# Kernel tuning notes

Measured on AMD Instinct MI355X. Metric: run time of the kernel, lower is better.

Reference implementation:

```python
import jax, jax.numpy as jnp
import numpy as np

EMBED_DIM = 128
NUM_SYMBOLS = 200000
B = 1024
K = 200
PROCESS_STEPS = 4


def setup_inputs() -> dict:
    key = jax.random.key(0)
    ks = jax.random.split(key, 10)
    D = EMBED_DIM
    emb = jax.random.normal(ks[0], (NUM_SYMBOLS + 1, D), jnp.float32) * 0.02
    emb = emb.at[NUM_SYMBOLS].set(0.0)  # padding_idx row
    return {
        "relations": jax.random.randint(ks[1], (B, K), 0, NUM_SYMBOLS),
        "entities": jax.random.randint(ks[2], (B, K), 0, NUM_SYMBOLS),
        "query": jax.random.randint(ks[3], (B,), 0, NUM_SYMBOLS),
        "symbol_emb": emb,
        "gcn_w_w": jax.random.normal(ks[4], (D, 2 * D), jnp.float32) / np.sqrt(2 * D).astype(np.float32),
        "gcn_w_b": jnp.zeros((D,), jnp.float32),
        "p1_w": jax.random.normal(ks[5], (2 * D, D), jnp.float32) / np.sqrt(D).astype(np.float32),
        "p1_b": jnp.zeros((2 * D,), jnp.float32),
        "p2_w": jax.random.normal(ks[6], (D, 2 * D), jnp.float32) / np.sqrt(2 * D).astype(np.float32),
        "p2_b": jnp.zeros((D,), jnp.float32),
        "ln_a": jnp.ones((D,), jnp.float32),
        "ln_b": jnp.zeros((D,), jnp.float32),
        "w_ih": jax.random.normal(ks[7], (8 * D, D), jnp.float32) * 0.05,
        "w_hh": jax.random.normal(ks[8], (8 * D, 2 * D), jnp.float32) * 0.05,
        "b_ih": jnp.zeros((8 * D,), jnp.float32),
        "b_hh": jnp.zeros((8 * D,), jnp.float32),
    }


def _layer_norm(z, a, b, eps=1e-3):
    # repo's LayerNormalization: (z - mu) / (std + eps) * a + b, unbiased std
    mu = jnp.mean(z, axis=-1, keepdims=True)
    sigma = jnp.std(z, axis=-1, ddof=1, keepdims=True)
    return (z - mu) / (sigma + eps) * a + b


def _forward(symbol_emb, gcn_w_w, gcn_w_b, p1_w, p1_b, p2_w, p2_b,
             ln_a, ln_b, w_ih, w_hh, b_ih, b_hh,
             relations, entities, query):
    D = symbol_emb.shape[1]
    # --- neighbor_encoder: gather -> concat -> linear -> neighbor sum -> tanh
    rel_e = symbol_emb[relations]                       # (B, K, D)
    ent_e = symbol_emb[entities]                        # (B, K, D)
    concat = jnp.concatenate([rel_e, ent_e], axis=-1)   # (B, K, 2D)
    out = jnp.einsum('bkf,df->bkd', concat, gcn_w_w) + gcn_w_b
    num_neighbors = jnp.asarray(relations.shape[0], out.dtype)  # code uses relations.size()[0]
    support = jnp.tanh(out.sum(axis=1) / num_neighbors)  # (B, D)
    # --- SupportEncoder: FFN with residual + layernorm (dropout off in eval)
    hidden = jax.nn.relu(support @ p1_w.T + p1_b)        # (B, 2D)
    support_g = _layer_norm(hidden @ p2_w.T + p2_b + support, ln_a, ln_b)
    # --- QueryEncoder: LSTMCell(D, 2D) process block with attention over support
    q = symbol_emb[query]                                # (B, D)
    bsz = q.shape[0]
    h_r = jnp.zeros((bsz, 2 * D), q.dtype)
    c = jnp.zeros((bsz, 2 * D), q.dtype)
    h_out = q
    for _ in range(PROCESS_STEPS):
        gates = q @ w_ih.T + b_ih + h_r @ w_hh.T + b_hh  # (B, 8D)
        i, f, g, o = jnp.split(gates, 4, axis=-1)
        c = jax.nn.sigmoid(f) * c + jax.nn.sigmoid(i) * jnp.tanh(g)
        h_ = jax.nn.sigmoid(o) * jnp.tanh(c)             # (B, 2D)
        h_out = q + h_[:, :D]                            # (B, D)
        attn = jax.nn.softmax(h_out @ support_g.T, axis=1)  # (B, B)
        r = attn @ support_g                             # (B, D)
        h_r = jnp.concatenate([h_out, r], axis=-1)       # (B, 2D)
    query_embeds = h_out
    # --- cosine similarity over dim=1
    cross = jnp.sum(query_embeds * support_g, axis=1)
    n1 = jnp.sum(query_embeds * query_embeds, axis=1)
    n2 = jnp.sum(support_g * support_g, axis=1)
    return cross / jnp.sqrt(n1 * n2)                     # (B,)


def reference(relations, entities, query, symbol_emb, gcn_w_w, gcn_w_b,
              p1_w, p1_b, p2_w, p2_b, ln_a, ln_b, w_ih, w_hh, b_ih, b_hh):
    return _forward(symbol_emb, gcn_w_w, gcn_w_b, p1_w, p1_b, p2_w, p2_b,
                    ln_a, ln_b, w_ih, w_hh, b_ih, b_hh,
                    relations, entities, query)
```

## Files before the change

### kernel.cpp

```cpp
#include <hip/hip_runtime.h>
#include <math.h>

#define D 128
#define B_SZ 1024
#define KNB 200
#define AW 392
#define SCW 1028
#define PW 1032

typedef _Float16 half8 __attribute__((ext_vector_type(8)));
typedef _Float16 half4 __attribute__((ext_vector_type(4)));
typedef float floatx4 __attribute__((ext_vector_type(4)));

__device__ __forceinline__ float sigmoid_f(float x) { return 1.f / (1.f + __expf(-x)); }
__device__ __forceinline__ float tanh_fast(float x) { return 1.f - 2.f / (__expf(2.f * x) + 1.f); }

__global__ __launch_bounds__(256) void k_prefetch(
    const float4* __restrict__ emb4, int n4, float* __restrict__ scratch)
{
    float s = 0.f;
    for (int i = blockIdx.x * 256 + threadIdx.x; i < n4; i += gridDim.x * 256) {
        float4 v = emb4[i];
        s += v.x + v.y + v.z + v.w;
    }
    for (int off = 32; off; off >>= 1) s += __shfl_down(s, off);
    if ((threadIdx.x & 63) == 0) scratch[blockIdx.x * 4 + (threadIdx.x >> 6)] = s;
}

__global__ __launch_bounds__(256) void k_cvtw(
    const float* __restrict__ w_ih, const float* __restrict__ w_hh,
    _Float16* __restrict__ w16)
{
    const int i8 = (blockIdx.x * 256 + threadIdx.x) * 8;
    const int row = i8 / 384, k = i8 % 384;
    const float* src = (k < 128) ? &w_ih[row * 128 + k] : &w_hh[row * 256 + (k - 128)];
    float4 v0 = *(const float4*)src;
    float4 v1 = *(const float4*)(src + 4);
    half8 h;
    h[0] = (_Float16)v0.x; h[1] = (_Float16)v0.y; h[2] = (_Float16)v0.z; h[3] = (_Float16)v0.w;
    h[4] = (_Float16)v1.x; h[5] = (_Float16)v1.y; h[6] = (_Float16)v1.z; h[7] = (_Float16)v1.w;
    *(half8*)&w16[i8] = h;
}

__global__ __launch_bounds__(512) void k_support(
    const int* __restrict__ relations, const int* __restrict__ entities,
    const int* __restrict__ query, const float* __restrict__ emb,
    const float* __restrict__ gcn_w, const float* __restrict__ gcn_b,
    const float* __restrict__ p1_w, const float* __restrict__ p1_b,
    const float* __restrict__ p2_w, const float* __restrict__ p2_b,
    const float* __restrict__ ln_a, const float* __restrict__ ln_b,
    float* __restrict__ sg, _Float16* __restrict__ sgH, _Float16* __restrict__ sgT,
    _Float16* __restrict__ qbH)
{
    __shared__ int idxs[2 * KNB];
    __shared__ __align__(16) float part[16][132];
    __shared__ __align__(16) float S[2 * D];
    __shared__ __align__(16) float sup[D];
    __shared__ __align__(16) float hid[2 * D];
    __shared__ __align__(16) float zv[D];
    __shared__ float red2[2];

    const int b = blockIdx.x;
    const int t = threadIdx.x;

    if (t < KNB) idxs[t] = relations[b * KNB + t];
    else if (t < 2 * KNB) idxs[t] = entities[b * KNB + (t - KNB)];
    __syncthreads();

    {
        const int g = t >> 5, c4 = (t & 31) * 4;
        const int* mi = &idxs[(g >> 3) * KNB];
        float4 a4 = make_float4(0.f, 0.f, 0.f, 0.f);
        #pragma unroll 5
        for (int k = (g & 7); k < KNB; k += 8) {
            float4 v = *(const float4*)&emb[(size_t)mi[k] * D + c4];
            a4.x += v.x; a4.y += v.y; a4.z += v.z; a4.w += v.w;
        }
        *(float4*)&part[g][c4] = a4;
    }
    __syncthreads();
    if (t < 2 * D) {
        const int half = t >> 7, c = t & 127;
        float s = 0.f;
        #pragma unroll
        for (int j = 0; j < 8; ++j) s += part[half * 8 + j][c];
        S[t] = s;
    }
    __syncthreads();

    if (t < D) {
        const float4* w4 = (const float4*)(gcn_w + t * 2 * D);
        float dot = 0.f;
        #pragma unroll 8
        for (int f = 0; f < 2 * D / 4; ++f) {
            float4 w = w4[f];
            float4 s = *(const float4*)&S[f * 4];
            dot += w.x * s.x + w.y * s.y + w.z * s.z + w.w * s.w;
        }
        float v = (dot + 200.f * gcn_b[t]) * (1.f / 1024.f);
        sup[t] = tanhf(v);
    }
    __syncthreads();

    if (t < 2 * D) {
        const float4* w4 = (const float4*)(p1_w + t * D);
        float dot = 0.f;
        #pragma unroll 8
        for (int f = 0; f < D / 4; ++f) {
            float4 w = w4[f];
            float4 s = *(const float4*)&sup[f * 4];
            dot += w.x * s.x + w.y * s.y + w.z * s.z + w.w * s.w;
        }
        float h = dot + p1_b[t];
        hid[t] = h > 0.f ? h : 0.f;
    }
    __syncthreads();

    if (t < D) {
        const float4* w4 = (const float4*)(p2_w + t * 2 * D);
        float dot = 0.f;
        #pragma unroll 8
        for (int f = 0; f < 2 * D / 4; ++f) {
            float4 w = w4[f];
            float4 s = *(const float4*)&hid[f * 4];
            dot += w.x * s.x + w.y * s.y + w.z * s.z + w.w * s.w;
        }
        zv[t] = dot + p2_b[t] + sup[t];
    }
    __syncthreads();

    if (t < 64) {
        float x0 = zv[t], x1 = zv[t + 64];
        float s = x0 + x1;
        for (int off = 32; off; off >>= 1) s += __shfl_down(s, off);
        float mu = __shfl(s, 0) * (1.f / 128.f);
        float d0 = x0 - mu, d1 = x1 - mu;
        float v = d0 * d0 + d1 * d1;
        for (int off = 32; off; off >>= 1) v += __shfl_down(v, off);
        v = __shfl(v, 0);
        if (t == 0) { red2[0] = mu; red2[1] = sqrtf(v * (1.f / 127.f)); }
    }
    __syncthreads();
    if (t < D) {
        float mu = red2[0], sigma = red2[1];
        float val = (zv[t] - mu) / (sigma + 1e-3f) * ln_a[t] + ln_b[t];
        sg[b * D + t] = val;
        sgH[b * D + t] = (_Float16)val;
        sgT[t * B_SZ + b] = (_Float16)val;
        qbH[b * D + t] = (_Float16)emb[(size_t)query[b] * D + t];
    }
}

__global__ __launch_bounds__(1024) void k_chain(
    const _Float16* __restrict__ qbH, const _Float16* __restrict__ sgH,
    const _Float16* __restrict__ sgT, const float* __restrict__ sg,
    const _Float16* __restrict__ w16, const float* __restrict__ b_ih,
    const float* __restrict__ b_hh, float* __restrict__ out)
{
    __shared__ _Float16 Ah[16 * AW];
    __shared__ float    Sc[16 * SCW];
    __shared__ _Float16 P[16 * PW];
    __shared__ float    sinv[16];
    __shared__ float    rpar[2][16][132];
    __shared__ float    hsave[16][132];

    const int t = threadIdx.x;
    const int wv = t >> 6, lane = t & 63;
    const int m = lane & 15, quad = lane >> 4;
    const int b0 = blockIdx.x * 16;

    if (t < 256) {
        const int row = t >> 4, ch = (t & 15) * 8;
        *(half8*)&Ah[row * AW + ch] = *(const half8*)&qbH[(b0 + row) * D + ch];
    }

    const int unit = wv * 16 + m;
    float bi[4];
    #pragma unroll
    for (int g = 0; g < 4; ++g) bi[g] = b_ih[g * 256 + unit] + b_hh[g * 256 + unit];

    floatx4 cfr;
    floatx4 gq[4];
    floatx4 acc[4];
    #pragma unroll
    for (int i = 0; i < 4; ++i) cfr[i] = 0.f;
    #pragma unroll
    for (int g = 0; g < 4; ++g)
        #pragma unroll
        for (int i = 0; i < 4; ++i) gq[g][i] = 0.f;

    __syncthreads();

    #pragma unroll
    for (int ks = 0; ks < 4; ++ks) {
        half8 a = *(const half8*)&Ah[m * AW + ks * 32 + quad * 8];
        #pragma unroll
        for (int g = 0; g < 4; ++g) {
            half8 bf = *(const half8*)&w16[(g * 256 + unit) * 384 + ks * 32 + quad * 8];
            gq[g] = __builtin_amdgcn_mfma_f32_16x16x32_f16(a, bf, gq[g], 0, 0, 0);
        }
    }

    auto gates_hr = [&]() {
        #pragma unroll
        for (int g = 0; g < 4; ++g) acc[g] = gq[g];
        #pragma unroll
        for (int ks = 0; ks < 8; ++ks) {
            half8 a = *(const half8*)&Ah[m * AW + 128 + ks * 32 + quad * 8];
            #pragma unroll
            for (int g = 0; g < 4; ++g) {
                half8 bf = *(const half8*)&w16[(g * 256 + unit) * 384 + 128 + ks * 32 + quad * 8];
                acc[g] = __builtin_amdgcn_mfma_f32_16x16x32_f16(a, bf, acc[g], 0, 0, 0);
            }
        }
    };

    auto pointwise = [&](bool first, bool save) {
        __syncthreads();
        #pragma unroll
        for (int rr = 0; rr < 4; ++rr) {
            float gi = acc[0][rr] + bi[0];
            float gf = acc[1][rr] + bi[1];
            float gg = acc[2][rr] + bi[2];
            float go = acc[3][rr] + bi[3];
            float cold = first ? 0.f : cfr[rr];
            float cn = sigmoid_f(gf) * cold + sigmoid_f(gi) * tanh_fast(gg);
            cfr[rr] = cn;
            if (wv < 8) {
                const int row = quad * 4 + rr;
                float qv = (float)Ah[row * AW + unit];
                float ho = qv + sigmoid_f(go) * tanh_fast(cn);
                Ah[row * AW + 128 + unit] = (_Float16)ho;
                if (save) hsave[row][unit] = ho;
            }
        }
    };

    auto attn = [&]() {
        __syncthreads();
        #pragma unroll
        for (int i = 0; i < 4; ++i) {
            const int j0 = (wv * 4 + i) * 16;
            floatx4 a2;
            #pragma unroll
            for (int z = 0; z < 4; ++z) a2[z] = 0.f;
            #pragma unroll
            for (int ks = 0; ks < 4; ++ks) {
                half8 a = *(const half8*)&Ah[m * AW + 128 + ks * 32 + quad * 8];
                half8 bf = *(const half8*)&sgH[(j0 + m) * D + ks * 32 + quad * 8];
                a2 = __builtin_amdgcn_mfma_f32_16x16x32_f16(a, bf, a2, 0, 0, 0);
            }
            #pragma unroll
            for (int rr = 0; rr < 4; ++rr)
                Sc[(quad * 4 + rr) * SCW + j0 + m] = a2[rr];
        }
        __syncthreads();
        {
            const int row = wv;
            float vals[16];
            float mm = -1e30f;
            #pragma unroll
            for (int j = 0; j < 16; ++j) {
                vals[j] = Sc[row * SCW + lane + j * 64];
                mm = fmaxf(mm, vals[j]);
            }
            #pragma unroll
            for (int off = 32; off; off >>= 1) mm = fmaxf(mm, __shfl_down(mm, off));
            mm = __shfl(mm, 0);
            float ss = 0.f;
            #pragma unroll
            for (int j = 0; j < 16; ++j) {
                float e = __expf(vals[j] - mm);
                P[row * PW + lane + j * 64] = (_Float16)e;
                ss += e;
            }
            #pragma unroll
            for (int off = 32; off; off >>= 1) ss += __shfl_down(ss, off);
            if (lane == 0) sinv[row] = 1.f / ss;
        }
        __syncthreads();
        {
            const int nt = wv & 7, kh = wv >> 3;
            floatx4 a3;
            #pragma unroll
            for (int z = 0; z < 4; ++z) a3[z] = 0.f;
            #pragma unroll
            for (int ks = 0; ks < 16; ++ks) {
                const int kk = kh * 16 + ks;
                half8 a = *(const half8*)&P[m * PW + kk * 32 + quad * 8];
                half8 bf = *(const half8*)&sgT[(nt * 16 + m) * B_SZ + kk * 32 + quad * 8];
                a3 = __builtin_amdgcn_mfma_f32_16x16x32_f16(a, bf, a3, 0, 0, 0);
            }
            #pragma unroll
            for (int rr = 0; rr < 4; ++rr)
                rpar[kh][quad * 4 + rr][nt * 16 + m] = a3[rr];
        }
        __syncthreads();
        #pragma unroll
        for (int e = t; e < 2048; e += 1024) {
            const int row = e >> 7, col = e & 127;
            float v = (rpar[0][row][col] + rpar[1][row][col]) * sinv[row];
            Ah[row * AW + 256 + col] = (_Float16)v;
        }
        __syncthreads();
    };

    #pragma unroll
    for (int g = 0; g < 4; ++g) acc[g] = gq[g];
    pointwise(true, false);
    attn();
    gates_hr(); pointwise(false, false); attn();
    gates_hr(); pointwise(false, false); attn();
    gates_hr(); pointwise(false, true);

    __syncthreads();
    if (t < 64) {
        const int row = t & 15, part = t >> 4;
        float cr = 0.f, n1 = 0.f, n2 = 0.f;
        #pragma unroll 8
        for (int j = 0; j < 32; ++j) {
            const int c = part * 32 + j;
            float h = hsave[row][c];
            float s = sg[(b0 + row) * D + c];
            cr += h * s; n1 += h * h; n2 += s * s;
        }
        cr += __shfl_down(cr, 16); n1 += __shfl_down(n1, 16); n2 += __shfl_down(n2, 16);
        cr += __shfl_down(cr, 32); n1 += __shfl_down(n1, 32); n2 += __shfl_down(n2, 32);
        if (t < 16) out[b0 + row] = cr / sqrtf(n1 * n2);
    }
}

extern "C" void kernel_launch(void* const* d_in, const int* in_sizes, int n_in,
                              void* d_out, int out_size, void* d_ws, size_t ws_size,
                              hipStream_t stream)
{
    const int*   relations = (const int*)d_in[0];
    const int*   entities  = (const int*)d_in[1];
    const int*   query     = (const int*)d_in[2];
    const float* emb       = (const float*)d_in[3];
    const float* gcn_w     = (const float*)d_in[4];
    const float* gcn_b     = (const float*)d_in[5];
    const float* p1_w      = (const float*)d_in[6];
    const float* p1_b      = (const float*)d_in[7];
    const float* p2_w      = (const float*)d_in[8];
    const float* p2_b      = (const float*)d_in[9];
    const float* ln_a      = (const float*)d_in[10];
    const float* ln_b      = (const float*)d_in[11];
    const float* w_ih      = (const float*)d_in[12];
    const float* w_hh      = (const float*)d_in[13];
    const float* b_ih      = (const float*)d_in[14];
    const float* b_hh      = (const float*)d_in[15];

    float* ws = (float*)d_ws;
    float*     sg      = ws;
    _Float16*  sgH     = (_Float16*)(ws + 131072);
    _Float16*  sgT     = (_Float16*)(ws + 196608);
    _Float16*  qbH     = (_Float16*)(ws + 262144);
    _Float16*  w16     = (_Float16*)(ws + 327680);
    float*     scratch = ws + 524288;

    const int n4 = (200001 * D) / 4;
    k_prefetch<<<dim3(2048), dim3(256), 0, stream>>>((const float4*)emb, n4, scratch);
    k_cvtw<<<dim3(192), dim3(256), 0, stream>>>(w_ih, w_hh, w16);
    k_support<<<dim3(B_SZ), dim3(512), 0, stream>>>(
        relations, entities, query, emb, gcn_w, gcn_b,
        p1_w, p1_b, p2_w, p2_b, ln_a, ln_b, sg, sgH, sgT, qbH);
    k_chain<<<dim3(64), dim3(1024), 0, stream>>>(
        qbH, sgH, sgT, sg, w16, b_ih, b_hh, (float*)d_out);
}
```

Measured before the change: 359.4 us.

## Split LSTM attention chain into per-step kernels and drop embedding prefetch

```diff
diff --git a/kernel.cpp b/kernel.cpp
--- a/kernel.cpp
+++ b/kernel.cpp
@@ -4,36 +4,23 @@
 #define D 128
 #define B_SZ 1024
 #define KNB 200
-#define AW 392
+#define QAW 136
+#define HAW 264
 #define SCW 1028
-#define PW 1032
+#define PW 1048
 
 typedef _Float16 half8 __attribute__((ext_vector_type(8)));
-typedef _Float16 half4 __attribute__((ext_vector_type(4)));
 typedef float floatx4 __attribute__((ext_vector_type(4)));
 
 __device__ __forceinline__ float sigmoid_f(float x) { return 1.f / (1.f + __expf(-x)); }
 __device__ __forceinline__ float tanh_fast(float x) { return 1.f - 2.f / (__expf(2.f * x) + 1.f); }
-
-__global__ __launch_bounds__(256) void k_prefetch(
-    const float4* __restrict__ emb4, int n4, float* __restrict__ scratch)
-{
-    float s = 0.f;
-    for (int i = blockIdx.x * 256 + threadIdx.x; i < n4; i += gridDim.x * 256) {
-        float4 v = emb4[i];
-        s += v.x + v.y + v.z + v.w;
-    }
-    for (int off = 32; off; off >>= 1) s += __shfl_down(s, off);
-    if ((threadIdx.x & 63) == 0) scratch[blockIdx.x * 4 + (threadIdx.x >> 6)] = s;
-}
 
 __global__ __launch_bounds__(256) void k_cvtw(
     const float* __restrict__ w_ih, const float* __restrict__ w_hh,
     _Float16* __restrict__ w16)
 {
     const int i8 = (blockIdx.x * 256 + threadIdx.x) * 8;
-    const int row = i8 / 384, k = i8 % 384;
-    const float* src = (k < 128) ? &w_ih[row * 128 + k] : &w_hh[row * 256 + (k - 128)];
+    const float* src = (i8 < 131072) ? (w_ih + i8) : (w_hh + (i8 - 131072));
     float4 v0 = *(const float4*)src;
     float4 v1 = *(const float4*)(src + 4);
     half8 h;
@@ -151,182 +138,236 @@
     }
 }
 
-__global__ __launch_bounds__(1024) void k_chain(
+__global__ __launch_bounds__(1024) void k_step(
     const _Float16* __restrict__ qbH, const _Float16* __restrict__ sgH,
     const _Float16* __restrict__ sgT, const float* __restrict__ sg,
     const _Float16* __restrict__ w16, const float* __restrict__ b_ih,
-    const float* __restrict__ b_hh, float* __restrict__ out)
+    const float* __restrict__ b_hh, float* __restrict__ gqB,
+    float* __restrict__ cbuf, _Float16* __restrict__ hH,
+    float* __restrict__ out, int first, int last)
 {
-    __shared__ _Float16 Ah[16 * AW];
+    __shared__ _Float16 qA[16 * QAW];
+    __shared__ _Float16 HA[16 * HAW];
     __shared__ float    Sc[16 * SCW];
     __shared__ _Float16 P[16 * PW];
+    __shared__ float    rpar[2][16][132];
     __shared__ float    sinv[16];
-    __shared__ float    rpar[2][16][132];
     __shared__ float    hsave[16][132];
 
     const int t = threadIdx.x;
     const int wv = t >> 6, lane = t & 63;
     const int m = lane & 15, quad = lane >> 4;
     const int b0 = blockIdx.x * 16;
+    const int u0 = wv * 16;
+    const int gg = m & 3;
+    const int base = lane & 60;
 
     if (t < 256) {
-        const int row = t >> 4, ch = (t & 15) * 8;
-        *(half8*)&Ah[row * AW + ch] = *(const half8*)&qbH[(b0 + row) * D + ch];
-    }
-
-    const int unit = wv * 16 + m;
-    float bi[4];
+        const int row = t >> 4, c = (t & 15) * 8;
+        *(half8*)&qA[row * QAW + c] = *(const half8*)&qbH[(b0 + row) * D + c];
+    }
+    if (!first && t >= 256 && t < 512) {
+        const int idx = t - 256;
+        const int row = idx >> 4, c = (idx & 15) * 8;
+        *(half8*)&HA[row * HAW + c] = *(const half8*)&hH[(b0 + row) * D + c];
+    }
+
+    int ucol[4], wrow[4];
     #pragma unroll
-    for (int g = 0; g < 4; ++g) bi[g] = b_ih[g * 256 + unit] + b_hh[g * 256 + unit];
-
-    floatx4 cfr;
-    floatx4 gq[4];
-    floatx4 acc[4];
-    #pragma unroll
-    for (int i = 0; i < 4; ++i) cfr[i] = 0.f;
-    #pragma unroll
-    for (int g = 0; g < 4; ++g)
-        #pragma unroll
-        for (int i = 0; i < 4; ++i) gq[g][i] = 0.f;
-
-    __syncthreads();
-
-    #pragma unroll
-    for (int ks = 0; ks < 4; ++ks) {
-        half8 a = *(const half8*)&Ah[m * AW + ks * 32 + quad * 8];
-        #pragma unroll
-        for (int g = 0; g < 4; ++g) {
-            half8 bf = *(const half8*)&w16[(g * 256 + unit) * 384 + ks * 32 + quad * 8];
-            gq[g] = __builtin_amdgcn_mfma_f32_16x16x32_f16(a, bf, gq[g], 0, 0, 0);
-        }
-    }
-
-    auto gates_hr = [&]() {
-        #pragma unroll
-        for (int g = 0; g < 4; ++g) acc[g] = gq[g];
-        #pragma unroll
-        for (int ks = 0; ks < 8; ++ks) {
-            half8 a = *(const half8*)&Ah[m * AW + 128 + ks * 32 + quad * 8];
-            #pragma unroll
-            for (int g = 0; g < 4; ++g) {
-                half8 bf = *(const half8*)&w16[(g * 256 + unit) * 384 + 128 + ks * 32 + quad * 8];
-                acc[g] = __builtin_amdgcn_mfma_f32_16x16x32_f16(a, bf, acc[g], 0, 0, 0);
-            }
-        }
-    };
-
-    auto pointwise = [&](bool first, bool save) {
-        __syncthreads();
-        #pragma unroll
-        for (int rr = 0; rr < 4; ++rr) {
-            float gi = acc[0][rr] + bi[0];
-            float gf = acc[1][rr] + bi[1];
-            float gg = acc[2][rr] + bi[2];
-            float go = acc[3][rr] + bi[3];
-            float cold = first ? 0.f : cfr[rr];
-            float cn = sigmoid_f(gf) * cold + sigmoid_f(gi) * tanh_fast(gg);
-            cfr[rr] = cn;
-            if (wv < 8) {
-                const int row = quad * 4 + rr;
-                float qv = (float)Ah[row * AW + unit];
-                float ho = qv + sigmoid_f(go) * tanh_fast(cn);
-                Ah[row * AW + 128 + unit] = (_Float16)ho;
-                if (save) hsave[row][unit] = ho;
-            }
-        }
-    };
-
-    auto attn = [&]() {
-        __syncthreads();
+    for (int j = 0; j < 4; ++j) { ucol[j] = u0 + j * 4 + (m >> 2); wrow[j] = gg * 256 + ucol[j]; }
+
+    float gqb[4][4];
+    float creg[4][4];
+    if (!first) {
+        #pragma unroll
+        for (int j = 0; j < 4; ++j)
+            #pragma unroll
+            for (int rr = 0; rr < 4; ++rr) {
+                const int b = b0 + quad * 4 + rr;
+                gqb[j][rr] = gqB[(size_t)b * 1024 + wrow[j]];
+                creg[j][rr] = cbuf[b * 256 + ucol[j]];
+            }
+    }
+    __syncthreads();
+
+    float qvr[4][4];
+    if (wv < 8) {
+        #pragma unroll
+        for (int j = 0; j < 4; ++j)
+            #pragma unroll
+            for (int rr = 0; rr < 4; ++rr)
+                qvr[j][rr] = (float)qA[(quad * 4 + rr) * QAW + ucol[j]];
+    }
+
+    if (first) {
+        floatx4 a0[4];
+        #pragma unroll
+        for (int j = 0; j < 4; ++j)
+            #pragma unroll
+            for (int z = 0; z < 4; ++z) a0[j][z] = 0.f;
+        #pragma unroll
+        for (int ks = 0; ks < 4; ++ks) {
+            half8 a = *(const half8*)&qA[m * QAW + ks * 32 + quad * 8];
+            #pragma unroll
+            for (int j = 0; j < 4; ++j) {
+                half8 bf = *(const half8*)&w16[wrow[j] * D + ks * 32 + quad * 8];
+                a0[j] = __builtin_amdgcn_mfma_f32_16x16x32_f16(a, bf, a0[j], 0, 0, 0);
+            }
+        }
+        #pragma unroll
+        for (int j = 0; j < 4; ++j) {
+            const float bv = b_ih[wrow[j]] + b_hh[wrow[j]];
+            #pragma unroll
+            for (int rr = 0; rr < 4; ++rr) {
+                gqb[j][rr] = a0[j][rr] + bv;
+                gqB[(size_t)(b0 + quad * 4 + rr) * 1024 + wrow[j]] = gqb[j][rr];
+            }
+        }
+        #pragma unroll
+        for (int j = 0; j < 4; ++j)
+            #pragma unroll
+            for (int rr = 0; rr < 4; ++rr) {
+                float v = gqb[j][rr];
+                float gi = __shfl(v, base + 0);
+                float ggt = __shfl(v, base + 2);
+                float go = __shfl(v, base + 3);
+                float cn = sigmoid_f(gi) * tanh_fast(ggt);
+                creg[j][rr] = cn;
+                if (wv < 8) {
+                    float ho = qvr[j][rr] + sigmoid_f(go) * tanh_fast(cn);
+                    if (gg == 0) HA[(quad * 4 + rr) * HAW + ucol[j]] = (_Float16)ho;
+                }
+            }
+    }
+    __syncthreads();
+
+    {
+        floatx4 s4[4];
+        #pragma unroll
+        for (int i = 0; i < 4; ++i)
+            #pragma unroll
+            for (int z = 0; z < 4; ++z) s4[i][z] = 0.f;
+        #pragma unroll
+        for (int ks = 0; ks < 4; ++ks) {
+            half8 a = *(const half8*)&HA[m * HAW + ks * 32 + quad * 8];
+            #pragma unroll
+            for (int i = 0; i < 4; ++i) {
+                const int j0 = (wv * 4 + i) * 16;
+                half8 bf = *(const half8*)&sgH[(j0 + m) * D + ks * 32 + quad * 8];
+                s4[i] = __builtin_amdgcn_mfma_f32_16x16x32_f16(a, bf, s4[i], 0, 0, 0);
+            }
+        }
         #pragma unroll
         for (int i = 0; i < 4; ++i) {
             const int j0 = (wv * 4 + i) * 16;
-            floatx4 a2;
-            #pragma unroll
-            for (int z = 0; z < 4; ++z) a2[z] = 0.f;
-            #pragma unroll
-            for (int ks = 0; ks < 4; ++ks) {
-                half8 a = *(const half8*)&Ah[m * AW + 128 + ks * 32 + quad * 8];
-                half8 bf = *(const half8*)&sgH[(j0 + m) * D + ks * 32 + quad * 8];
-                a2 = __builtin_amdgcn_mfma_f32_16x16x32_f16(a, bf, a2, 0, 0, 0);
-            }
             #pragma unroll
             for (int rr = 0; rr < 4; ++rr)
-                Sc[(quad * 4 + rr) * SCW + j0 + m] = a2[rr];
-        }
+                Sc[(quad * 4 + rr) * SCW + j0 + m] = s4[i][rr];
+        }
+    }
+    __syncthreads();
+    {
+        const int row = wv;
+        float vals[16];
+        float mm = -1e30f;
+        #pragma unroll
+        for (int j = 0; j < 16; ++j) {
+            vals[j] = Sc[row * SCW + lane + j * 64];
+            mm = fmaxf(mm, vals[j]);
+        }
+        #pragma unroll
+        for (int off = 32; off; off >>= 1) mm = fmaxf(mm, __shfl_down(mm, off));
+        mm = __shfl(mm, 0);
+        float ss = 0.f;
+        #pragma unroll
+        for (int j = 0; j < 16; ++j) {
+            float e = __expf(vals[j] - mm);
+            P[row * PW + lane + j * 64] = (_Float16)e;
+            ss += e;
+        }
+        #pragma unroll
+        for (int off = 32; off; off >>= 1) ss += __shfl_down(ss, off);
+        if (lane == 0) sinv[row] = 1.f / ss;
+    }
+    __syncthreads();
+    {
+        const int nt = wv & 7, kh = wv >> 3;
+        floatx4 a3;
+        #pragma unroll
+        for (int z = 0; z < 4; ++z) a3[z] = 0.f;
+        #pragma unroll
+        for (int ks = 0; ks < 16; ++ks) {
+            const int kk = kh * 16 + ks;
+            half8 a = *(const half8*)&P[m * PW + kk * 32 + quad * 8];
+            half8 bf = *(const half8*)&sgT[(nt * 16 + m) * B_SZ + kk * 32 + quad * 8];
+            a3 = __builtin_amdgcn_mfma_f32_16x16x32_f16(a, bf, a3, 0, 0, 0);
+        }
+        #pragma unroll
+        for (int rr = 0; rr < 4; ++rr)
+            rpar[kh][quad * 4 + rr][nt * 16 + m] = a3[rr];
+    }
+    __syncthreads();
+    for (int e = t; e < 2048; e += 1024) {
+        const int row = e >> 7, col = e & 127;
+        float v = (rpar[0][row][col] + rpar[1][row][col]) * sinv[row];
+        HA[row * HAW + 128 + col] = (_Float16)v;
+    }
+    __syncthreads();
+
+    {
+        floatx4 ac[4];
+        #pragma unroll
+        for (int j = 0; j < 4; ++j)
+            #pragma unroll
+            for (int rr = 0; rr < 4; ++rr) ac[j][rr] = gqb[j][rr];
+        #pragma unroll
+        for (int ks = 0; ks < 8; ++ks) {
+            half8 a = *(const half8*)&HA[m * HAW + ks * 32 + quad * 8];
+            #pragma unroll
+            for (int j = 0; j < 4; ++j) {
+                half8 bf = *(const half8*)&w16[131072 + wrow[j] * 256 + ks * 32 + quad * 8];
+                ac[j] = __builtin_amdgcn_mfma_f32_16x16x32_f16(a, bf, ac[j], 0, 0, 0);
+            }
+        }
+        #pragma unroll
+        for (int j = 0; j < 4; ++j)
+            #pragma unroll
+            for (int rr = 0; rr < 4; ++rr) {
+                float v = ac[j][rr];
+                float gi = __shfl(v, base + 0);
+                float gf = __shfl(v, base + 1);
+                float ggt = __shfl(v, base + 2);
+                float go = __shfl(v, base + 3);
+                float cn = sigmoid_f(gf) * creg[j][rr] + sigmoid_f(gi) * tanh_fast(ggt);
+                creg[j][rr] = cn;
+                const int b = b0 + quad * 4 + rr;
+                if (!last && gg == 0) cbuf[b * 256 + ucol[j]] = cn;
+                if (wv < 8) {
+                    float ho = qvr[j][rr] + sigmoid_f(go) * tanh_fast(cn);
+                    if (gg == 0) {
+                        if (!last) hH[b * D + ucol[j]] = (_Float16)ho;
+                        else       hsave[quad * 4 + rr][ucol[j]] = ho;
+                    }
+                }
+            }
+    }
+
+    if (last) {
         __syncthreads();
-        {
-            const int row = wv;
-            float vals[16];
-            float mm = -1e30f;
-            #pragma unroll
-            for (int j = 0; j < 16; ++j) {
-                vals[j] = Sc[row * SCW + lane + j * 64];
-                mm = fmaxf(mm, vals[j]);
-            }
-            #pragma unroll
-            for (int off = 32; off; off >>= 1) mm = fmaxf(mm, __shfl_down(mm, off));
-            mm = __shfl(mm, 0);
-            float ss = 0.f;
-            #pragma unroll
-            for (int j = 0; j < 16; ++j) {
-                float e = __expf(vals[j] - mm);
-                P[row * PW + lane + j * 64] = (_Float16)e;
-                ss += e;
-            }
-            #pragma unroll
-            for (int off = 32; off; off >>= 1) ss += __shfl_down(ss, off);
-            if (lane == 0) sinv[row] = 1.f / ss;
-        }
-        __syncthreads();
-        {
-            const int nt = wv & 7, kh = wv >> 3;
-            floatx4 a3;
-            #pragma unroll
-            for (int z = 0; z < 4; ++z) a3[z] = 0.f;
-            #pragma unroll
-            for (int ks = 0; ks < 16; ++ks) {
-                const int kk = kh * 16 + ks;
-                half8 a = *(const half8*)&P[m * PW + kk * 32 + quad * 8];
-                half8 bf = *(const half8*)&sgT[(nt * 16 + m) * B_SZ + kk * 32 + quad * 8];
-                a3 = __builtin_amdgcn_mfma_f32_16x16x32_f16(a, bf, a3, 0, 0, 0);
-            }
-            #pragma unroll
-            for (int rr = 0; rr < 4; ++rr)
-                rpar[kh][quad * 4 + rr][nt * 16 + m] = a3[rr];
-        }
-        __syncthreads();
-        #pragma unroll
-        for (int e = t; e < 2048; e += 1024) {
-            const int row = e >> 7, col = e & 127;
-            float v = (rpar[0][row][col] + rpar[1][row][col]) * sinv[row];
-            Ah[row * AW + 256 + col] = (_Float16)v;
-        }
-        __syncthreads();
-    };
-
-    #pragma unroll
-    for (int g = 0; g < 4; ++g) acc[g] = gq[g];
-    pointwise(true, false);
-    attn();
-    gates_hr(); pointwise(false, false); attn();
-    gates_hr(); pointwise(false, false); attn();
-    gates_hr(); pointwise(false, true);
-
-    __syncthreads();
-    if (t < 64) {
-        const int row = t & 15, part = t >> 4;
-        float cr = 0.f, n1 = 0.f, n2 = 0.f;
-        #pragma unroll 8
-        for (int j = 0; j < 32; ++j) {
-            const int c = part * 32 + j;
-            float h = hsave[row][c];
-            float s = sg[(b0 + row) * D + c];
-            cr += h * s; n1 += h * h; n2 += s * s;
-        }
-        cr += __shfl_down(cr, 16); n1 += __shfl_down(n1, 16); n2 += __shfl_down(n2, 16);
-        cr += __shfl_down(cr, 32); n1 += __shfl_down(n1, 32); n2 += __shfl_down(n2, 32);
-        if (t < 16) out[b0 + row] = cr / sqrtf(n1 * n2);
+        if (t < 64) {
+            const int row = t & 15, part = t >> 4;
+            float cr = 0.f, n1 = 0.f, n2 = 0.f;
+            #pragma unroll 8
+            for (int j = 0; j < 32; ++j) {
+                const int c = part * 32 + j;
+                float h = hsave[row][c];
+                float s = sg[(b0 + row) * D + c];
+                cr += h * s; n1 += h * h; n2 += s * s;
+            }
+            cr += __shfl_down(cr, 16); n1 += __shfl_down(n1, 16); n2 += __shfl_down(n2, 16);
+            cr += __shfl_down(cr, 32); n1 += __shfl_down(n1, 32); n2 += __shfl_down(n2, 32);
+            if (t < 16) out[b0 + row] = cr / sqrtf(n1 * n2);
+        }
     }
 }
 
@@ -352,19 +393,24 @@
     const float* b_hh      = (const float*)d_in[15];
 
     float* ws = (float*)d_ws;
-    float*     sg      = ws;
-    _Float16*  sgH     = (_Float16*)(ws + 131072);
-    _Float16*  sgT     = (_Float16*)(ws + 196608);
-    _Float16*  qbH     = (_Float16*)(ws + 262144);
-    _Float16*  w16     = (_Float16*)(ws + 327680);
-    float*     scratch = ws + 524288;
-
-    const int n4 = (200001 * D) / 4;
-    k_prefetch<<<dim3(2048), dim3(256), 0, stream>>>((const float4*)emb, n4, scratch);
+    float*     sg   = ws;
+    _Float16*  sgH  = (_Float16*)(ws + 131072);
+    _Float16*  sgT  = (_Float16*)(ws + 196608);
+    _Float16*  qbH  = (_Float16*)(ws + 262144);
+    _Float16*  hH   = (_Float16*)(ws + 327680);
+    float*     cb   = ws + 393216;
+    float*     gqB  = ws + 655360;
+    _Float16*  w16  = (_Float16*)(ws + 1703936);
+
     k_cvtw<<<dim3(192), dim3(256), 0, stream>>>(w_ih, w_hh, w16);
     k_support<<<dim3(B_SZ), dim3(512), 0, stream>>>(
         relations, entities, query, emb, gcn_w, gcn_b,
         p1_w, p1_b, p2_w, p2_b, ln_a, ln_b, sg, sgH, sgT, qbH);
-    k_chain<<<dim3(64), dim3(1024), 0, stream>>>(
-        qbH, sgH, sgT, sg, w16, b_ih, b_hh, (float*)d_out);
+
+    k_step<<<dim3(64), dim3(1024), 0, stream>>>(
+        qbH, sgH, sgT, sg, w16, b_ih, b_hh, gqB, cb, hH, (float*)d_out, 1, 0);
+    k_step<<<dim3(64), dim3(1024), 0, stream>>>(
+        qbH, sgH, sgT, sg, w16, b_ih, b_hh, gqB, cb, hH, (float*)d_out, 0, 0);
+    k_step<<<dim3(64), dim3(1024), 0, stream>>>(
+        qbH, sgH, sgT, sg, w16, b_ih, b_hh, gqB, cb, hH, (float*)d_out, 0, 1);
 }
```

Result: faster. 351.5 us (-2.2%).
